# Optimization experiments

Measured on AMD Instinct MI355X. Metric: run time of the kernel, lower is better.

Reference implementation:

```python
import jax, jax.numpy as jnp
import numpy as np

EPS_NORM = 1e-12   # F.normalize eps
EPS_PERP = 1e-10   # perplexity log eps
COMMIT = 0.25


def _l2norm(x):
    # matches F.normalize(p=2, dim=1) with eps clamp
    n = jnp.sqrt(jnp.sum(x * x, axis=1, keepdims=True))
    return x / jnp.maximum(n, EPS_NORM)


def setup_inputs() -> dict:
    key = jax.random.key(0)
    k1, k2 = jax.random.split(key)
    B, D, L, K = 8, 256, 4096, 4096
    inputs = jax.random.normal(k1, (B, D, L), dtype=jnp.float32)
    # nn.Embedding init uniform(-1/K, 1/K); use uniform at that scale
    weight = jax.random.uniform(k2, (K, D), minval=-1.0 / K, maxval=1.0 / K, dtype=jnp.float32)
    return {"inputs": inputs, "weight": weight}


def reference(inputs, weight):
    K, D = weight.shape
    x = jnp.transpose(inputs, (0, 2, 1))          # [B, L, D]
    flat = x.reshape(-1, D)                       # [N, D]
    N = flat.shape[0]
    sim = _l2norm(flat) @ _l2norm(weight).T       # [N, K] cosine similarity
    # argmin(1 - sim) == argmax(sim)
    idx = jnp.argmax(sim, axis=1)                 # [N]
    # one-hot @ weight is just a gather of the selected code rows
    quantized = weight[idx].reshape(x.shape)      # [B, L, D]
    e_latent = jnp.mean((jax.lax.stop_gradient(quantized) - x) ** 2)
    q_latent = jnp.mean((quantized - jax.lax.stop_gradient(x)) ** 2)
    loss = q_latent + COMMIT * e_latent
    # straight-through estimator
    q_st = x + jax.lax.stop_gradient(quantized - x)
    # avg_probs = mean of one-hot encodings = normalized histogram of idx
    counts = jnp.zeros((K,), dtype=jnp.float32).at[idx].add(1.0)
    avg_probs = counts / N
    perplexity = jnp.exp(-jnp.sum(avg_probs * jnp.log(avg_probs + EPS_PERP)))
    return jnp.transpose(q_st, (0, 2, 1)), loss, perplexity
```

## Files before the change

kernel.cpp:

```cpp
#include <hip/hip_runtime.h>
#include <stdint.h>

#define Bb 8
#define Dd 256
#define Ll 4096
#define Kk 4096
#define Nn (Bb * Ll)
#define OUT0 (Bb * Dd * Ll)

typedef int    int4v   __attribute__((ext_vector_type(4)));
typedef int    int8v   __attribute__((ext_vector_type(8)));
typedef float  floatx4 __attribute__((ext_vector_type(4)));

#define SCALE1 0x7F7F7F7F

union V8 { int8v v; int4v h[2]; };

__device__ __forceinline__ void async_load16(const void* g, void* l) {
    __builtin_amdgcn_global_load_lds((const __attribute__((address_space(1))) void*)g,
                                     (__attribute__((address_space(3))) void*)l, 16, 0, 0);
}

__global__ void k_prep(const float* __restrict__ w, unsigned char* __restrict__ wn,
                       int* __restrict__ counts) {
    int blk = blockIdx.x, tid = threadIdx.x;
    if (blk == 0)
        for (int i = tid; i < Kk + 2; i += 256) counts[i] = 0;
    int row  = blk * 4 + (tid >> 6);
    int lane = tid & 63;
    float4 v = ((const float4*)(w + (size_t)row * Dd))[lane];
    float ss = v.x*v.x + v.y*v.y + v.z*v.z + v.w*v.w;
#pragma unroll
    for (int m = 1; m < 64; m <<= 1) ss += __shfl_xor(ss, m, 64);
    float s = 16.0f / fmaxf(sqrtf(ss), 1e-12f);
    int p = __builtin_amdgcn_cvt_pk_fp8_f32(v.x * s, v.y * s, 0, false);
    p     = __builtin_amdgcn_cvt_pk_fp8_f32(v.z * s, v.w * s, p, true);
    ((int*)(wn + (size_t)row * Dd))[lane] = p;
}

__global__ __launch_bounds__(512, 2) void k_gemm_argmax(
        const float* __restrict__ x, const unsigned char* __restrict__ Wn,
        int* __restrict__ idxout) {
    __shared__ __align__(16) unsigned char As[128 * 256];
    __shared__ __align__(16) unsigned char Bs[2][128 * 256];
    __shared__ unsigned int red[128][4];

    int bm = blockIdx.x;
    int tid = threadIdx.x, lane = tid & 63, w = tid >> 6;
    int wm = w >> 2, wn = w & 3;
    int l15 = lane & 15, l4 = lane >> 4;

    int goff[4], loff[4];
#pragma unroll
    for (int j = 0; j < 4; ++j) {
        int q = j * 512 + tid;
        int col = q >> 4, p = q & 15;
        goff[j] = col * 256 + ((p ^ (col & 15)) << 4);
        loff[j] = q * 16;
    }

#pragma unroll
    for (int j = 0; j < 4; ++j)
        async_load16(Wn + goff[j], (unsigned char*)Bs[0] + loff[j]);

    int b = bm >> 5, l0 = (bm & 31) * 128;
    const float* xs = x + (size_t)b * Dd * Ll + l0;
    int lg = tid & 31, dgr = tid >> 5;
#pragma unroll
    for (int i = 0; i < 4; ++i) {
        int d0 = dgr * 4 + i * 64;
        const float* s0 = xs + (size_t)d0 * Ll + lg * 4;
        float4 f0 = *(const float4*)(s0);
        float4 f1 = *(const float4*)(s0 + Ll);
        float4 f2 = *(const float4*)(s0 + 2 * (size_t)Ll);
        float4 f3 = *(const float4*)(s0 + 3 * (size_t)Ll);
#pragma unroll
        for (int jl = 0; jl < 4; ++jl) {
            float a0 = ((const float*)&f0)[jl], a1 = ((const float*)&f1)[jl];
            float a2 = ((const float*)&f2)[jl], a3 = ((const float*)&f3)[jl];
            int pk = __builtin_amdgcn_cvt_pk_fp8_f32(a0, a1, 0, false);
            pk     = __builtin_amdgcn_cvt_pk_fp8_f32(a2, a3, pk, true);
            int l = lg * 4 + jl;
            *(int*)(As + l * 256 + (((d0 >> 4) ^ (l & 15)) << 4) + (d0 & 15)) = pk;
        }
    }
    __syncthreads();

    int8v af[4][2];
#pragma unroll
    for (int fm = 0; fm < 4; ++fm)
#pragma unroll
        for (int ks = 0; ks < 2; ++ks) {
            int l = wm * 64 + fm * 16 + l15;
            int ch = ks * 8 + l4 * 2;
            V8 u;
            u.h[0] = *(const int4v*)(As + l * 256 + ((ch ^ l15) << 4));
            u.h[1] = *(const int4v*)(As + l * 256 + (((ch + 1) ^ l15) << 4));
            af[fm][ks] = u.v;
        }

    unsigned int rk[4][4];
#pragma unroll
    for (int fm = 0; fm < 4; ++fm)
#pragma unroll
        for (int r = 0; r < 4; ++r) rk[fm][r] = 0u;

    for (int cb = 0; cb < 32; ++cb) {
        int cur = cb & 1;
        if (cb < 31) {
            const unsigned char* g = Wn + (size_t)(cb + 1) * 128 * 256;
            unsigned char* lb = (unsigned char*)Bs[cur ^ 1];
#pragma unroll
            for (int j = 0; j < 4; ++j)
                async_load16(g + goff[j], lb + loff[j]);
        }
        const unsigned char* bb = (const unsigned char*)Bs[cur];
        int8v bf[2][2];
#pragma unroll
        for (int fn = 0; fn < 2; ++fn)
#pragma unroll
            for (int ks = 0; ks < 2; ++ks) {
                int col = wn * 32 + fn * 16 + l15;
                int ch = ks * 8 + l4 * 2;
                V8 u;
                u.h[0] = *(const int4v*)(bb + col * 256 + ((ch ^ l15) << 4));
                u.h[1] = *(const int4v*)(bb + col * 256 + (((ch + 1) ^ l15) << 4));
                bf[fn][ks] = u.v;
            }
        floatx4 acc[4][2];
#pragma unroll
        for (int fm = 0; fm < 4; ++fm)
#pragma unroll
            for (int fn = 0; fn < 2; ++fn) {
                floatx4 a = (floatx4)512.0f;
                a = __builtin_amdgcn_mfma_scale_f32_16x16x128_f8f6f4(
                        af[fm][0], bf[fn][0], a, 0, 0, 0, SCALE1, 0, SCALE1);
                a = __builtin_amdgcn_mfma_scale_f32_16x16x128_f8f6f4(
                        af[fm][1], bf[fn][1], a, 0, 0, 0, SCALE1, 0, SCALE1);
                acc[fm][fn] = a;
            }
        unsigned int i0 = (unsigned)(cb * 128 + wn * 32 + l15);
#pragma unroll
        for (int fm = 0; fm < 4; ++fm)
#pragma unroll
            for (int r = 0; r < 4; ++r) {
                unsigned int k0 = (__float_as_uint(acc[fm][0][r]) & 0xFFFFF000u) | i0;
                unsigned int k1 = (__float_as_uint(acc[fm][1][r]) & 0xFFFFF000u) | (i0 + 16u);
                unsigned int km = k0 > k1 ? k0 : k1;
                rk[fm][r] = rk[fm][r] > km ? rk[fm][r] : km;
            }
        __syncthreads();
    }

#pragma unroll
    for (int fm = 0; fm < 4; ++fm)
#pragma unroll
        for (int r = 0; r < 4; ++r) {
            unsigned int kx = rk[fm][r];
#pragma unroll
            for (int md = 1; md <= 8; md <<= 1) {
                unsigned int o = (unsigned int)__shfl_xor((int)kx, md, 64);
                kx = kx > o ? kx : o;
            }
            if (l15 == 0) red[wm * 64 + fm * 16 + l4 * 4 + r][wn] = kx;
        }
    __syncthreads();
    if (tid < 128) {
        unsigned int k0 = red[tid][0], k1 = red[tid][1];
        unsigned int k2 = red[tid][2], k3 = red[tid][3];
        unsigned int kx = k0 > k1 ? k0 : k1;
        kx = kx > k2 ? kx : k2;
        kx = kx > k3 ? kx : k3;
        idxout[bm * 128 + tid] = (int)(kx & 0xFFFu);
    }
}

__global__ __launch_bounds__(256) void k_gather(
        const float* __restrict__ w, const float* __restrict__ x,
        const int* __restrict__ idx, float* __restrict__ out,
        int* __restrict__ counts) {
    __shared__ float wt[128 * 65];
    __shared__ int kidx[128];
    __shared__ float wsum[4];
    __shared__ int lastsh;
    float* lossacc = (float*)(counts + Kk);
    int*   done    = counts + Kk + 1;

    int blk = blockIdx.x, tid = threadIdx.x;
    int dq = blk & 3, lb = blk >> 2;
    int n0 = lb * 128;
    if (tid < 128) {
        int ix = idx[n0 + tid];
        kidx[tid] = ix;
        if (dq == 0) atomicAdd(&counts[ix], 1);
    }
    __syncthreads();
    int lane = tid & 63, wv = tid >> 6;
    {
        int rr = lane >> 4, c16 = lane & 15;
#pragma unroll
        for (int jr = 0; jr < 8; ++jr) {
            int r = wv * 32 + jr * 4 + rr;
            float4 v = *(const float4*)(w + (size_t)kidx[r] * Dd + dq * 64 + c16 * 4);
            float* dst = &wt[r * 65 + c16 * 4];
            dst[0] = v.x; dst[1] = v.y; dst[2] = v.z; dst[3] = v.w;
        }
    }
    __syncthreads();

    int lq = tid & 31, dg = tid >> 5;
    int b = n0 >> 12, l0 = n0 & (Ll - 1);
    const float* xp = x   + ((size_t)b * Dd + dq * 64) * Ll + l0 + lq * 4;
    float*       op = out + ((size_t)b * Dd + dq * 64) * Ll + l0 + lq * 4;
    int r0 = lq * 4;
    float ls = 0.f;
#pragma unroll
    for (int i = 0; i < 8; ++i) {
        int d = i * 8 + dg;
        float4 xv = *(const float4*)(xp + (size_t)d * Ll);
        float4 qv = { wt[r0 * 65 + d],       wt[(r0 + 1) * 65 + d],
                      wt[(r0 + 2) * 65 + d], wt[(r0 + 3) * 65 + d] };
        float d0 = qv.x - xv.x, d1 = qv.y - xv.y, d2 = qv.z - xv.z, d3 = qv.w - xv.w;
        ls += d0*d0 + d1*d1 + d2*d2 + d3*d3;
        *(float4*)(op + (size_t)d * Ll) = qv;
    }
#pragma unroll
    for (int m = 1; m < 64; m <<= 1) ls += __shfl_xor(ls, m, 64);
    if (lane == 0) wsum[wv] = ls;
    __syncthreads();
    if (tid == 0) {
        atomicAdd(lossacc, wsum[0] + wsum[1] + wsum[2] + wsum[3]);
        __threadfence();
        lastsh = (atomicAdd(done, 1) == 1023);
    }
    __syncthreads();
    if (lastsh) {
        __threadfence();
        float s = 0.f;
        for (int i = tid; i < Kk; i += 256) {
            float p = (float)counts[i] * (1.0f / Nn);
            s += p * logf(p + 1e-10f);
        }
#pragma unroll
        for (int m = 1; m < 64; m <<= 1) s += __shfl_xor(s, m, 64);
        if (lane == 0) wsum[wv] = s;
        __syncthreads();
        if (tid == 0) {
            out[OUT0]     = lossacc[0] * 1.25f / (float)OUT0;
            out[OUT0 + 1] = expf(-(wsum[0] + wsum[1] + wsum[2] + wsum[3]));
        }
    }
}

extern "C" void kernel_launch(void* const* d_in, const int* in_sizes, int n_in,
                              void* d_out, int out_size, void* d_ws, size_t ws_size,
                              hipStream_t stream) {
    const float* x = (const float*)d_in[0];
    const float* w = (const float*)d_in[1];
    float* out = (float*)d_out;
    char* ws = (char*)d_ws;

    unsigned char* wn   = (unsigned char*)ws;
    int*           idx  = (int*)(ws + (1u << 20));
    int*           counts = (int*)(ws + (1u << 20) + (128u << 10));

    k_prep       <<<1024, 256, 0, stream>>>(w, wn, counts);
    k_gemm_argmax<<<256,  512, 0, stream>>>(x, wn, idx);
    k_gather     <<<1024, 256, 0, stream>>>(w, x, idx, out, counts);
}
```

Baseline: 176.7 us.

## Fuse gather, loss and histogram epilogue into the GEMM-argmax kernel

Folds the separate gather kernel into the GEMM/argmax kernel's epilogue. The winning indices stay in shared memory, the codebook rows are staged through a shared buffer that aliases the GEMM tiles, and x is re-read to compute the loss and write the output. This removes one launch and the idx round trip through global memory. In exchange, only 256 blocks now do the bandwidth-bound output write, so parallelism and latency hiding in that phase drop, and the epilogue is serialized after the GEMM in each block.

After: 150.1 us. 15.1% less time.

```diff
diff --git a/kernel.cpp b/kernel.cpp
--- a/kernel.cpp
+++ b/kernel.cpp
@@ -38,16 +38,26 @@
     ((int*)(wn + (size_t)row * Dd))[lane] = p;
 }
 
-__global__ __launch_bounds__(512, 2) void k_gemm_argmax(
+__global__ __launch_bounds__(512, 2) void k_gemm_fused(
         const float* __restrict__ x, const unsigned char* __restrict__ Wn,
-        int* __restrict__ idxout) {
-    __shared__ __align__(16) unsigned char As[128 * 256];
-    __shared__ __align__(16) unsigned char Bs[2][128 * 256];
+        const float* __restrict__ w, float* __restrict__ out,
+        int* __restrict__ counts) {
+    union Smem {
+        struct { unsigned char As[128 * 256]; unsigned char Bs[2][128 * 256]; } g;
+        float wt[64 * 260];
+    };
+    __shared__ __align__(16) Smem sm;
     __shared__ unsigned int red[128][4];
+    __shared__ int kidx[128];
+    __shared__ float wsum[8];
+    __shared__ int lastsh;
+
+    float* lossacc = (float*)(counts + Kk);
+    int*   done    = counts + Kk + 1;
 
     int bm = blockIdx.x;
-    int tid = threadIdx.x, lane = tid & 63, w = tid >> 6;
-    int wm = w >> 2, wn = w & 3;
+    int tid = threadIdx.x, lane = tid & 63, wv = tid >> 6;
+    int wm = wv >> 2, wn = wv & 3;
     int l15 = lane & 15, l4 = lane >> 4;
 
     int goff[4], loff[4];
@@ -61,7 +71,7 @@
 
 #pragma unroll
     for (int j = 0; j < 4; ++j)
-        async_load16(Wn + goff[j], (unsigned char*)Bs[0] + loff[j]);
+        async_load16(Wn + goff[j], (unsigned char*)sm.g.Bs[0] + loff[j]);
 
     int b = bm >> 5, l0 = (bm & 31) * 128;
     const float* xs = x + (size_t)b * Dd * Ll + l0;
@@ -81,7 +91,7 @@
             int pk = __builtin_amdgcn_cvt_pk_fp8_f32(a0, a1, 0, false);
             pk     = __builtin_amdgcn_cvt_pk_fp8_f32(a2, a3, pk, true);
             int l = lg * 4 + jl;
-            *(int*)(As + l * 256 + (((d0 >> 4) ^ (l & 15)) << 4) + (d0 & 15)) = pk;
+            *(int*)(sm.g.As + l * 256 + (((d0 >> 4) ^ (l & 15)) << 4) + (d0 & 15)) = pk;
         }
     }
     __syncthreads();
@@ -94,8 +104,8 @@
             int l = wm * 64 + fm * 16 + l15;
             int ch = ks * 8 + l4 * 2;
             V8 u;
-            u.h[0] = *(const int4v*)(As + l * 256 + ((ch ^ l15) << 4));
-            u.h[1] = *(const int4v*)(As + l * 256 + (((ch + 1) ^ l15) << 4));
+            u.h[0] = *(const int4v*)(sm.g.As + l * 256 + ((ch ^ l15) << 4));
+            u.h[1] = *(const int4v*)(sm.g.As + l * 256 + (((ch + 1) ^ l15) << 4));
             af[fm][ks] = u.v;
         }
 
@@ -109,12 +119,12 @@
         int cur = cb & 1;
         if (cb < 31) {
             const unsigned char* g = Wn + (size_t)(cb + 1) * 128 * 256;
-            unsigned char* lb = (unsigned char*)Bs[cur ^ 1];
+            unsigned char* lb = (unsigned char*)sm.g.Bs[cur ^ 1];
 #pragma unroll
             for (int j = 0; j < 4; ++j)
                 async_load16(g + goff[j], lb + loff[j]);
         }
-        const unsigned char* bb = (const unsigned char*)Bs[cur];
+        const unsigned char* bb = (const unsigned char*)sm.g.Bs[cur];
         int8v bf[2][2];
 #pragma unroll
         for (int fn = 0; fn < 2; ++fn)
@@ -171,73 +181,60 @@
         unsigned int kx = k0 > k1 ? k0 : k1;
         kx = kx > k2 ? kx : k2;
         kx = kx > k3 ? kx : k3;
-        idxout[bm * 128 + tid] = (int)(kx & 0xFFFu);
-    }
-}
-
-__global__ __launch_bounds__(256) void k_gather(
-        const float* __restrict__ w, const float* __restrict__ x,
-        const int* __restrict__ idx, float* __restrict__ out,
-        int* __restrict__ counts) {
-    __shared__ float wt[128 * 65];
-    __shared__ int kidx[128];
-    __shared__ float wsum[4];
-    __shared__ int lastsh;
-    float* lossacc = (float*)(counts + Kk);
-    int*   done    = counts + Kk + 1;
-
-    int blk = blockIdx.x, tid = threadIdx.x;
-    int dq = blk & 3, lb = blk >> 2;
-    int n0 = lb * 128;
-    if (tid < 128) {
-        int ix = idx[n0 + tid];
+        int ix = (int)(kx & 0xFFFu);
         kidx[tid] = ix;
-        if (dq == 0) atomicAdd(&counts[ix], 1);
-    }
-    __syncthreads();
-    int lane = tid & 63, wv = tid >> 6;
-    {
-        int rr = lane >> 4, c16 = lane & 15;
-#pragma unroll
-        for (int jr = 0; jr < 8; ++jr) {
-            int r = wv * 32 + jr * 4 + rr;
-            float4 v = *(const float4*)(w + (size_t)kidx[r] * Dd + dq * 64 + c16 * 4);
-            float* dst = &wt[r * 65 + c16 * 4];
-            dst[0] = v.x; dst[1] = v.y; dst[2] = v.z; dst[3] = v.w;
-        }
-    }
-    __syncthreads();
-
-    int lq = tid & 31, dg = tid >> 5;
-    int b = n0 >> 12, l0 = n0 & (Ll - 1);
-    const float* xp = x   + ((size_t)b * Dd + dq * 64) * Ll + l0 + lq * 4;
-    float*       op = out + ((size_t)b * Dd + dq * 64) * Ll + l0 + lq * 4;
-    int r0 = lq * 4;
+        atomicAdd(&counts[ix], 1);
+    }
+    __syncthreads();
+
     float ls = 0.f;
-#pragma unroll
-    for (int i = 0; i < 8; ++i) {
-        int d = i * 8 + dg;
-        float4 xv = *(const float4*)(xp + (size_t)d * Ll);
-        float4 qv = { wt[r0 * 65 + d],       wt[(r0 + 1) * 65 + d],
-                      wt[(r0 + 2) * 65 + d], wt[(r0 + 3) * 65 + d] };
-        float d0 = qv.x - xv.x, d1 = qv.y - xv.y, d2 = qv.z - xv.z, d3 = qv.w - xv.w;
-        ls += d0*d0 + d1*d1 + d2*d2 + d3*d3;
-        *(float4*)(op + (size_t)d * Ll) = qv;
-    }
+    int fl = tid & 15, dg = tid >> 4;
+    size_t xbase = (size_t)b * Dd * Ll + l0 + fl * 4;
+    for (int h = 0; h < 2; ++h) {
+        float4 xv[8];
+        size_t hb = xbase + h * 64;
+#pragma unroll
+        for (int p = 0; p < 8; ++p)
+            xv[p] = *(const float4*)(x + hb + (size_t)(p * 32 + dg) * Ll);
+
+        int rr = tid >> 3, c8 = tid & 7;
+        const float* src = w + (size_t)kidx[h * 64 + rr] * Dd + c8 * 4;
+        float4 vv[8];
+#pragma unroll
+        for (int j = 0; j < 8; ++j) vv[j] = *(const float4*)(src + j * 32);
+#pragma unroll
+        for (int j = 0; j < 8; ++j)
+            *(float4*)&sm.wt[rr * 260 + (c8 + j * 8) * 4] = vv[j];
+        __syncthreads();
+
+#pragma unroll
+        for (int p = 0; p < 8; ++p) {
+            int d = p * 32 + dg;
+            float4 qv = { sm.wt[(fl * 4 + 0) * 260 + d], sm.wt[(fl * 4 + 1) * 260 + d],
+                          sm.wt[(fl * 4 + 2) * 260 + d], sm.wt[(fl * 4 + 3) * 260 + d] };
+            float d0 = qv.x - xv[p].x, d1 = qv.y - xv[p].y;
+            float d2 = qv.z - xv[p].z, d3 = qv.w - xv[p].w;
+            ls += d0 * d0 + d1 * d1 + d2 * d2 + d3 * d3;
+            *(float4*)(out + hb + (size_t)d * Ll) = qv;
+        }
+        __syncthreads();
+    }
+
 #pragma unroll
     for (int m = 1; m < 64; m <<= 1) ls += __shfl_xor(ls, m, 64);
     if (lane == 0) wsum[wv] = ls;
     __syncthreads();
     if (tid == 0) {
-        atomicAdd(lossacc, wsum[0] + wsum[1] + wsum[2] + wsum[3]);
+        atomicAdd(lossacc, wsum[0] + wsum[1] + wsum[2] + wsum[3]
+                         + wsum[4] + wsum[5] + wsum[6] + wsum[7]);
         __threadfence();
-        lastsh = (atomicAdd(done, 1) == 1023);
+        lastsh = (atomicAdd(done, 1) == 255);
     }
     __syncthreads();
     if (lastsh) {
         __threadfence();
         float s = 0.f;
-        for (int i = tid; i < Kk; i += 256) {
+        for (int i = tid; i < Kk; i += 512) {
             float p = (float)counts[i] * (1.0f / Nn);
             s += p * logf(p + 1e-10f);
         }
@@ -247,7 +244,8 @@
         __syncthreads();
         if (tid == 0) {
             out[OUT0]     = lossacc[0] * 1.25f / (float)OUT0;
-            out[OUT0 + 1] = expf(-(wsum[0] + wsum[1] + wsum[2] + wsum[3]));
+            out[OUT0 + 1] = expf(-(wsum[0] + wsum[1] + wsum[2] + wsum[3]
+                                 + wsum[4] + wsum[5] + wsum[6] + wsum[7]));
         }
     }
 }
@@ -260,11 +258,9 @@
     float* out = (float*)d_out;
     char* ws = (char*)d_ws;
 
-    unsigned char* wn   = (unsigned char*)ws;
-    int*           idx  = (int*)(ws + (1u << 20));
-    int*           counts = (int*)(ws + (1u << 20) + (128u << 10));
-
-    k_prep       <<<1024, 256, 0, stream>>>(w, wn, counts);
-    k_gemm_argmax<<<256,  512, 0, stream>>>(x, wn, idx);
-    k_gather     <<<1024, 256, 0, stream>>>(w, x, idx, out, counts);
-}
+    unsigned char* wn     = (unsigned char*)ws;
+    int*           counts = (int*)(ws + (1u << 20));
+
+    k_prep      <<<1024, 256, 0, stream>>>(w, wn, counts);
+    k_gemm_fused<<<256,  512, 0, stream>>>(x, wn, w, out, counts);
+}
```
